# Optimization experiments

Measured on AMD Instinct MI355X. Metric: run time of the kernel, lower is better.

The kernel has to match this reference:

```python
import jax, jax.numpy as jnp
import numpy as np

N_NODES = 50000
N_EDGES = 800000
D_IN = 128
HIDDEN = 128
N_GRAPHS = 64


def gcn_conv(x, src, dst, W, b, num_nodes):
    """PyG GCNConv: out = D^{-1/2} (A+I) D^{-1/2} (x W) + b.
    src/dst already include self-loops."""
    h = x @ W  # [N, out]
    deg = jax.ops.segment_sum(jnp.ones_like(dst, dtype=h.dtype), dst,
                              num_segments=num_nodes)  # in-degree incl. self loop
    dinv = jnp.where(deg > 0, jax.lax.rsqrt(jnp.maximum(deg, 1e-12)), 0.0)
    norm = dinv[src] * dinv[dst]  # [E+N]
    msgs = h[src] * norm[:, None]  # gather + scale
    out = jax.ops.segment_sum(msgs, dst, num_segments=num_nodes)
    return out + b


def setup_inputs() -> dict:
    key = jax.random.key(0)
    ks = jax.random.split(key, 8)
    x = jax.random.normal(ks[0], (N_NODES, D_IN), dtype=jnp.float32)
    edge_index = jax.random.randint(ks[1], (2, N_EDGES), 0, N_NODES, dtype=jnp.int64)
    batch = jnp.sort(jax.random.randint(ks[2], (N_NODES,), 0, N_GRAPHS, dtype=jnp.int64))
    # Glorot-ish scaled params
    s = lambda fan_in: 1.0 / np.sqrt(fan_in)
    W1 = jax.random.normal(ks[3], (D_IN, HIDDEN), dtype=jnp.float32) * s(D_IN)
    b1 = jnp.zeros((HIDDEN,), dtype=jnp.float32)
    W2 = jax.random.normal(ks[4], (HIDDEN, HIDDEN), dtype=jnp.float32) * s(HIDDEN)
    b2 = jnp.zeros((HIDDEN,), dtype=jnp.float32)
    Wh1 = jax.random.normal(ks[5], (HIDDEN, HIDDEN), dtype=jnp.float32) * s(HIDDEN)
    bh1 = jnp.zeros((HIDDEN,), dtype=jnp.float32)
    Wh2 = jax.random.normal(ks[6], (HIDDEN, 1), dtype=jnp.float32) * s(HIDDEN)
    bh2 = jnp.zeros((1,), dtype=jnp.float32)
    return {"x": x, "edge_index": edge_index, "batch": batch,
            "W1": W1, "b1": b1, "W2": W2, "b2": b2,
            "Wh1": Wh1, "bh1": bh1, "Wh2": Wh2, "bh2": bh2}


def reference(x, edge_index, batch, W1, b1, W2, b2, Wh1, bh1, Wh2, bh2):
    n = x.shape[0]
    loop = jnp.arange(n, dtype=edge_index.dtype)
    src = jnp.concatenate([edge_index[0], loop])  # add self-loops once
    dst = jnp.concatenate([edge_index[1], loop])
    h = jax.nn.relu(gcn_conv(x, src, dst, W1, b1, n))
    h = jax.nn.relu(gcn_conv(h, src, dst, W2, b2, n))
    # global mean pool over graphs
    sums = jax.ops.segment_sum(h, batch, num_segments=N_GRAPHS)
    cnts = jax.ops.segment_sum(jnp.ones((n,), dtype=h.dtype), batch,
                               num_segments=N_GRAPHS)
    pooled = sums / jnp.maximum(cnts, 1.0)[:, None]  # [G, HIDDEN]
    # MLP head: Linear -> ReLU -> Linear -> Sigmoid -> squeeze(-1)
    z = jax.nn.relu(pooled @ Wh1 + bh1)
    out = jax.nn.sigmoid(z @ Wh2 + bh2)
    return out[:, 0]  # [G]
```

## Files before the change

### kernel.cpp

```cpp
#include <hip/hip_runtime.h>


#define NB 256
#define NBK 256

typedef __attribute__((ext_vector_type(8))) short bf16x8;
typedef __attribute__((ext_vector_type(4))) float f32x4;
typedef __attribute__((ext_vector_type(2))) float f32x2;

__device__ inline unsigned short f2bf(float f) {
    union { float f; unsigned int u; } c; c.f = f;
    unsigned int u = c.u + (0x7fffu + ((c.u >> 16) & 1u));
    return (unsigned short)(u >> 16);
}
__device__ inline float bf2f(unsigned short b) {
    union { unsigned int u; float f; } c; c.u = ((unsigned int)b) << 16;
    return c.f;
}

__device__ inline unsigned char f2fp8_sw(float f) {
    union { float f; unsigned int u; } c; c.f = f;
    unsigned int s = (c.u >> 24) & 0x80u;
    unsigned int au = c.u & 0x7FFFFFFFu;
    if (au >= 0x3C800000u) {
        if (au > 0x43E00000u) au = 0x43E00000u;
        unsigned int r = au + 0x000FFFFFu + ((au >> 20) & 1u);
        unsigned int e8 = (r >> 23) - 120u;
        unsigned int m8 = (r >> 20) & 7u;
        return (unsigned char)(s | (e8 << 3) | m8);
    }
    float av = c.f < 0.f ? -c.f : c.f;
    unsigned int M = (unsigned int)(av * 512.0f + 0.5f);
    return (unsigned char)(s | M);
}
__device__ inline float fp82f_sw(unsigned int cbyte) {
    unsigned int E = (cbyte >> 3) & 0xFu, M = cbyte & 7u;
    union { unsigned int u; float f; } v;
    v.u = ((E + 120u) << 23) | (M << 20);
    float r = E ? v.f : (float)M * 0.001953125f;
    return (cbyte & 0x80u) ? -r : r;
}

template <bool HI>
__device__ inline f32x2 fp8x2_f32(unsigned int u) {
#if __has_builtin(__builtin_amdgcn_cvt_pk_f32_fp8)
    return __builtin_amdgcn_cvt_pk_f32_fp8(u, HI);
#else
    unsigned int w = HI ? (u >> 16) : u;
    f32x2 r; r[0] = fp82f_sw(w & 0xFFu); r[1] = fp82f_sw((w >> 8) & 0xFFu);
    return r;
#endif
}
__device__ inline unsigned char f2fp8(float f) {
#if __has_builtin(__builtin_amdgcn_cvt_pk_fp8_f32)
    return (unsigned char)(__builtin_amdgcn_cvt_pk_fp8_f32(f, f, 0, false) & 0xFFu);
#else
    return f2fp8_sw(f);
#endif
}

__global__ __launch_bounds__(256) void k_hist(const int* __restrict__ dst,
                                              int* __restrict__ hist,
                                              float* __restrict__ sums,
                                              float* __restrict__ cnt,
                                              int ne, int chunk) {
    __shared__ int h[NBK];
    int t = threadIdx.x, b = blockIdx.x;
    h[t] = 0;
    int gid = b * 256 + t;
    if (gid < 64 * 128) sums[gid] = 0.0f;
    if (gid < 64) cnt[gid] = 0.0f;
    __syncthreads();
    int e0 = b * chunk, e1 = min(e0 + chunk, ne);
    for (int e = e0 + t; e < e1; e += 256) atomicAdd(&h[dst[e] >> 8], 1);
    __syncthreads();
    hist[b * NBK + t] = h[t];
}

__global__ __launch_bounds__(256) void k_scanb(int* __restrict__ hist,
                                               int* __restrict__ bstart,
                                               int* __restrict__ row_start,
                                               int n, int ne) {
    __shared__ int ps[256];
    int j = threadIdx.x;
    int run = 0;
    for (int i = 0; i < NB; ++i) {
        int t = hist[i * NBK + j];
        hist[i * NBK + j] = run;
        run += t;
    }
    ps[j] = run;
    __syncthreads();
    for (int off = 1; off < 256; off <<= 1) {
        int v = (j >= off) ? ps[j - off] : 0;
        __syncthreads();
        ps[j] += v;
        __syncthreads();
    }
    int excl = ps[j] - run;
    bstart[j] = excl;
    if (j == 255) bstart[256] = ps[255];
    if (j == 0) row_start[n] = ne;
    for (int i = 0; i < NB; ++i) hist[i * NBK + j] += excl;
}

__global__ __launch_bounds__(256) void k_scat(const int* __restrict__ src,
                                              const int* __restrict__ dst,
                                              const int* __restrict__ hist,
                                              unsigned int* __restrict__ ebuf,
                                              int ne, int chunk) {
    __shared__ int cur[NBK];
    int t = threadIdx.x, b = blockIdx.x;
    cur[t] = hist[b * NBK + t];
    __syncthreads();
    int e0 = b * chunk, e1 = min(e0 + chunk, ne);
    for (int e = e0 + t; e < e1; e += 256) {
        int d = dst[e];
        int p = atomicAdd(&cur[d >> 8], 1);
        ebuf[p] = ((unsigned int)(d & 255) << 24) | (unsigned int)src[e];
    }
}

__global__ __launch_bounds__(256) void k_bsort(const unsigned int* __restrict__ ebuf,
                                               const int* __restrict__ bstart,
                                               int* __restrict__ csr,
                                               int* __restrict__ row_start,
                                               float* __restrict__ dinv,
                                               int n) {
    __shared__ int h[NBK];
    __shared__ int sc[NBK];
    int j = threadIdx.x, b = blockIdx.x;
    int s0 = bstart[b], s1 = bstart[b + 1];
    h[j] = 0;
    __syncthreads();
    for (int e = s0 + j; e < s1; e += 256) atomicAdd(&h[ebuf[e] >> 24], 1);
    __syncthreads();
    sc[j] = h[j];
    __syncthreads();
    for (int off = 1; off < 256; off <<= 1) {
        int v = (j >= off) ? sc[j - off] : 0;
        __syncthreads();
        sc[j] += v;
        __syncthreads();
    }
    int excl = sc[j] - h[j];
    int id = b * 256 + j;
    int deg = h[j];
    if (id < n) {
        row_start[id] = s0 + excl;
        dinv[id] = rsqrtf((float)deg + 1.0f);
    }
    __syncthreads();
    h[j] = excl;
    __syncthreads();
    for (int e = s0 + j; e < s1; e += 256) {
        unsigned int pk = ebuf[e];
        int p = atomicAdd(&h[pk >> 24], 1);
        csr[s0 + p] = (int)(pk & 0x00FFFFFFu);
    }
}

__global__ __launch_bounds__(256) void k_castw(const float* __restrict__ W1,
                                               const float* __restrict__ W2,
                                               unsigned short* __restrict__ Wt1,
                                               unsigned short* __restrict__ Wt2) {
    int tid = blockIdx.x * 256 + threadIdx.x;
    int i = tid & 16383;
    int nn = i >> 7, kk = i & 127;
    if (tid < 16384) Wt1[i] = f2bf(W1[kk * 128 + nn]);
    else             Wt2[i] = f2bf(W2[kk * 128 + nn]);
}

template <bool F32IN>
__global__ __launch_bounds__(256) void k_gemm_mfma(const void* __restrict__ Xin,
                                                   const short* __restrict__ Wt,
                                                   unsigned char* __restrict__ Y8,
                                                   int n_rows) {
    int wid = threadIdx.x >> 6;
    int lane = threadIdx.x & 63;
    int r = lane & 15, q = lane >> 4;
    int m0 = blockIdx.x * 64;
    int n0 = wid * 32;

    bf16x8 bfr[2][4];
#pragma unroll
    for (int nt = 0; nt < 2; ++nt)
#pragma unroll
        for (int ks = 0; ks < 4; ++ks)
            bfr[nt][ks] = *(const bf16x8*)(Wt + (size_t)(n0 + nt * 16 + r) * 128 +
                                           ks * 32 + q * 8);

#pragma unroll
    for (int rt = 0; rt < 4; ++rt) {
        int row = m0 + rt * 16 + r;
        int rl = min(row, n_rows - 1);
        f32x4 acc0 = {0.f, 0.f, 0.f, 0.f};
        f32x4 acc1 = {0.f, 0.f, 0.f, 0.f};
#pragma unroll
        for (int ks = 0; ks < 4; ++ks) {
            bf16x8 a;
            if constexpr (F32IN) {
                const float* xr = (const float*)Xin + (size_t)rl * 128 + ks * 32 + q * 8;
                float4 f0 = *(const float4*)xr;
                float4 f1 = *(const float4*)(xr + 4);
                a[0] = (short)f2bf(f0.x); a[1] = (short)f2bf(f0.y);
                a[2] = (short)f2bf(f0.z); a[3] = (short)f2bf(f0.w);
                a[4] = (short)f2bf(f1.x); a[5] = (short)f2bf(f1.y);
                a[6] = (short)f2bf(f1.z); a[7] = (short)f2bf(f1.w);
            } else {
                a = *(const bf16x8*)((const short*)Xin + (size_t)rl * 128 + ks * 32 + q * 8);
            }
            acc0 = __builtin_amdgcn_mfma_f32_16x16x32_bf16(a, bfr[0][ks], acc0, 0, 0, 0);
            acc1 = __builtin_amdgcn_mfma_f32_16x16x32_bf16(a, bfr[1][ks], acc1, 0, 0, 0);
        }
#pragma unroll
        for (int v = 0; v < 4; ++v) {
            int orow = m0 + rt * 16 + q * 4 + v;
            if (orow < n_rows) {
                Y8[(size_t)orow * 128 + n0 + r]      = f2fp8(acc0[v]);
                Y8[(size_t)orow * 128 + n0 + 16 + r] = f2fp8(acc1[v]);
            }
        }
    }
}

__global__ __launch_bounds__(256) void k_agg(const unsigned char* __restrict__ h8,
                                             const float* __restrict__ dinv,
                                             const int* __restrict__ csr,
                                             const int* __restrict__ row_start,
                                             const float* __restrict__ bias,
                                             unsigned short* __restrict__ out,
                                             int n) {
    int node = blockIdx.x * 4 + (threadIdx.x >> 6);
    if (node >= n) return;
    int lane = threadIdx.x & 63;
    int s = lane >> 5, fi = lane & 31;
    const unsigned int* hp = (const unsigned int*)h8;

    float di = dinv[node];
    float selfw = (s == 0) ? di * di : 0.0f;
    unsigned int hu = hp[(size_t)node * 32 + fi];
    f32x2 p0 = fp8x2_f32<false>(hu);
    f32x2 p1 = fp8x2_f32<true>(hu);
    float a0 = p0[0] * selfw, a1 = p0[1] * selfw;
    float a2 = p1[0] * selfw, a3 = p1[1] * selfw;

    int beg = row_start[node];
    int end = row_start[node + 1];
    int deg = end - beg;

    int mysrc = (lane < deg) ? csr[beg + lane] : 0;
    float myw = ((lane < deg) ? dinv[mysrc] : 0.0f) * di;

    int m = min(deg, 64);
    int e = 0;
    for (; e + 8 <= m; e += 8) {
        int i0 = e + s, i1 = e + 2 + s, i2 = e + 4 + s, i3 = e + 6 + s;
        int s0 = __shfl(mysrc, i0);
        int s1 = __shfl(mysrc, i1);
        int s2 = __shfl(mysrc, i2);
        int s3 = __shfl(mysrc, i3);
        float w0 = __shfl(myw, i0);
        float w1 = __shfl(myw, i1);
        float w2 = __shfl(myw, i2);
        float w3 = __shfl(myw, i3);
        unsigned int u0 = hp[(size_t)s0 * 32 + fi];
        unsigned int u1 = hp[(size_t)s1 * 32 + fi];
        unsigned int u2 = hp[(size_t)s2 * 32 + fi];
        unsigned int u3 = hp[(size_t)s3 * 32 + fi];
        f32x2 v;
        v = fp8x2_f32<false>(u0); a0 += v[0] * w0; a1 += v[1] * w0;
        v = fp8x2_f32<true>(u0);  a2 += v[0] * w0; a3 += v[1] * w0;
        v = fp8x2_f32<false>(u1); a0 += v[0] * w1; a1 += v[1] * w1;
        v = fp8x2_f32<true>(u1);  a2 += v[0] * w1; a3 += v[1] * w1;
        v = fp8x2_f32<false>(u2); a0 += v[0] * w2; a1 += v[1] * w2;
        v = fp8x2_f32<true>(u2);  a2 += v[0] * w2; a3 += v[1] * w2;
        v = fp8x2_f32<false>(u3); a0 += v[0] * w3; a1 += v[1] * w3;
        v = fp8x2_f32<true>(u3);  a2 += v[0] * w3; a3 += v[1] * w3;
    }
    for (; e < m; e += 2) {
        int idx = e + s;
        int sx = __shfl(mysrc, idx & 63);
        float w = __shfl(myw, idx & 63);
        if (idx >= m) w = 0.0f;
        unsigned int u = hp[(size_t)sx * 32 + fi];
        f32x2 v;
        v = fp8x2_f32<false>(u); a0 += v[0] * w; a1 += v[1] * w;
        v = fp8x2_f32<true>(u);  a2 += v[0] * w; a3 += v[1] * w;
    }
    if (s == 0) {
        for (int j = beg + 64; j < end; ++j) {
            int sx = csr[j];
            float w = dinv[sx] * di;
            unsigned int u = hp[(size_t)sx * 32 + fi];
            f32x2 v;
            v = fp8x2_f32<false>(u); a0 += v[0] * w; a1 += v[1] * w;
            v = fp8x2_f32<true>(u);  a2 += v[0] * w; a3 += v[1] * w;
        }
    }

    a0 += __shfl_xor(a0, 32);
    a1 += __shfl_xor(a1, 32);
    a2 += __shfl_xor(a2, 32);
    a3 += __shfl_xor(a3, 32);

    if (s == 0) {
        float4 bv = ((const float4*)bias)[fi];
        float o0 = fmaxf(a0 + bv.x, 0.0f);
        float o1 = fmaxf(a1 + bv.y, 0.0f);
        float o2 = fmaxf(a2 + bv.z, 0.0f);
        float o3 = fmaxf(a3 + bv.w, 0.0f);
        uint2 pk;
        pk.x = (unsigned int)f2bf(o0) | ((unsigned int)f2bf(o1) << 16);
        pk.y = (unsigned int)f2bf(o2) | ((unsigned int)f2bf(o3) << 16);
        *(uint2*)(out + (size_t)node * 128 + fi * 4) = pk;
    }
}

#define POOL_CHUNK 64
__global__ __launch_bounds__(128) void k_pool(const unsigned short* __restrict__ h,
                                              const int* __restrict__ batch,
                                              float* __restrict__ sums,
                                              float* __restrict__ cnt, int n) {
    int d = threadIdx.x;
    int c0 = blockIdx.x * POOL_CHUNK;
    if (c0 >= n) return;
    int c1 = min(c0 + POOL_CHUNK, n);
    float acc = 0.f, cc = 0.f;
    int g_cur = batch[c0];
    for (int i = c0; i < c1; ++i) {
        int g = batch[i];
        if (g != g_cur) {
            atomicAdd(&sums[g_cur * 128 + d], acc);
            if (d == 0) atomicAdd(&cnt[g_cur], cc);
            acc = 0.f; cc = 0.f; g_cur = g;
        }
        acc += bf2f(h[(size_t)i * 128 + d]);
        cc += 1.f;
    }
    atomicAdd(&sums[g_cur * 128 + d], acc);
    if (d == 0) atomicAdd(&cnt[g_cur], cc);
}

__global__ __launch_bounds__(128) void k_head(const float* __restrict__ sums,
                                              const float* __restrict__ cnt,
                                              const float* __restrict__ Wh1,
                                              const float* __restrict__ bh1,
                                              const float* __restrict__ Wh2,
                                              const float* __restrict__ bh2,
                                              float* __restrict__ out) {
    int g = blockIdx.x;
    int d = threadIdx.x;
    __shared__ float sp[128];
    __shared__ float red[128];
    float c = fmaxf(cnt[g], 1.0f);
    sp[d] = sums[g * 128 + d] / c;
    __syncthreads();
    float acc = bh1[d];
    for (int k = 0; k < 128; ++k) acc += sp[k] * Wh1[k * 128 + d];
    float z = fmaxf(acc, 0.f);
    red[d] = z * Wh2[d];
    __syncthreads();
    for (int off = 64; off > 0; off >>= 1) {
        if (d < off) red[d] += red[d + off];
        __syncthreads();
    }
    if (d == 0) out[g] = 1.f / (1.f + expf(-(red[0] + bh2[0])));
}

extern "C" void kernel_launch(void* const* d_in, const int* in_sizes, int n_in,
                              void* d_out, int out_size, void* d_ws,
                              size_t ws_size, hipStream_t stream) {
    const float* x    = (const float*)d_in[0];
    const int*   ei   = (const int*)d_in[1];
    const int*   batch= (const int*)d_in[2];
    const float* W1   = (const float*)d_in[3];
    const float* b1   = (const float*)d_in[4];
    const float* W2   = (const float*)d_in[5];
    const float* b2   = (const float*)d_in[6];
    const float* Wh1  = (const float*)d_in[7];
    const float* bh1  = (const float*)d_in[8];
    const float* Wh2  = (const float*)d_in[9];
    const float* bh2  = (const float*)d_in[10];
    float* out = (float*)d_out;

    const int n  = in_sizes[0] / 128;
    const int ne = in_sizes[1] / 2;
    const int* src = ei;
    const int* dst = ei + ne;

    char* p = (char*)d_ws;
    int* hist      = (int*)p;  p += (size_t)NB * NBK * 4;
    int* bstart    = (int*)p;  p += 257 * 4;
    int* row_start = (int*)p;  p += (size_t)(n + 1) * 4;
    float* dinv    = (float*)p; p += (size_t)n * 4;
    unsigned int* ebuf = (unsigned int*)p; p += (size_t)ne * 4;
    int* csr       = (int*)p;  p += (size_t)ne * 4;
    p = (char*)(((uintptr_t)p + 15) & ~(uintptr_t)15);
    unsigned short* Wt1 = (unsigned short*)p; p += 128 * 128 * 2;
    unsigned short* Wt2 = (unsigned short*)p; p += 128 * 128 * 2;
    unsigned char* h8   = (unsigned char*)p; p += (size_t)n * 128;
    p = (char*)(((uintptr_t)p + 15) & ~(uintptr_t)15);
    unsigned short* abf = (unsigned short*)p; p += (size_t)n * 128 * 2;
    p = (char*)(((uintptr_t)p + 15) & ~(uintptr_t)15);
    float* sums = (float*)p;   p += (size_t)64 * 128 * 4;
    float* cnt  = (float*)p;

    int chunk = (ne + NB - 1) / NB;
    int nb_g = (n + 63) / 64;
    int nb_a = (n + 3) / 4;
    int nb_p = (n + POOL_CHUNK - 1) / POOL_CHUNK;

    k_hist<<<NB, 256, 0, stream>>>(dst, hist, sums, cnt, ne, chunk);
    k_scanb<<<1, 256, 0, stream>>>(hist, bstart, row_start, n, ne);
    k_scat<<<NB, 256, 0, stream>>>(src, dst, hist, ebuf, ne, chunk);
    k_bsort<<<256, 256, 0, stream>>>(ebuf, bstart, csr, row_start, dinv, n);

    k_castw<<<128, 256, 0, stream>>>(W1, W2, Wt1, Wt2);

    k_gemm_mfma<true><<<nb_g, 256, 0, stream>>>((const void*)x, (const short*)Wt1, h8, n);
    k_agg<<<nb_a, 256, 0, stream>>>(h8, dinv, csr, row_start, b1, abf, n);

    k_gemm_mfma<false><<<nb_g, 256, 0, stream>>>((const void*)abf, (const short*)Wt2, h8, n);
    k_agg<<<nb_a, 256, 0, stream>>>(h8, dinv, csr, row_start, b2, abf, n);

    k_pool<<<nb_p, 128, 0, stream>>>(abf, batch, sums, cnt, n);
    k_head<<<64, 128, 0, stream>>>(sums, cnt, Wh1, bh1, Wh2, bh2, out);
}
```

Measured before the change: 182.4 us.

## Fuse weight cast into histogram, pool into head, and pack shuffle payloads

Folds the bf16 weight transpose-cast into the histogram kernel and merges mean-pooling with the MLP head into a single per-graph kernel. The fused kernel finds each graph's node range by binary search over the sorted batch array, which removes two launches and the global atomics and zero-init of the sums buffers. The aggregation kernel now packs the source index (16 bits) and the bf16-rounded edge weight into one word, so each neighbour needs one shuffle instead of two. In exchange, node indices must fit in 16 bits, edge weights lose precision, and pooling runs on only 64 blocks, each walking its graph's rows serially.

```diff
diff --git a/kernel.cpp b/kernel.cpp
--- a/kernel.cpp
+++ b/kernel.cpp
@@ -16,6 +16,9 @@
 __device__ inline float bf2f(unsigned short b) {
     union { unsigned int u; float f; } c; c.u = ((unsigned int)b) << 16;
     return c.f;
+}
+__device__ inline float asf(unsigned int u) {
+    union { unsigned int u; float f; } c; c.u = u; return c.f;
 }
 
 __device__ inline unsigned char f2fp8_sw(float f) {
@@ -61,15 +64,22 @@
 
 __global__ __launch_bounds__(256) void k_hist(const int* __restrict__ dst,
                                               int* __restrict__ hist,
-                                              float* __restrict__ sums,
-                                              float* __restrict__ cnt,
+                                              const float* __restrict__ W1,
+                                              const float* __restrict__ W2,
+                                              unsigned short* __restrict__ Wt1,
+                                              unsigned short* __restrict__ Wt2,
                                               int ne, int chunk) {
     __shared__ int h[NBK];
     int t = threadIdx.x, b = blockIdx.x;
     h[t] = 0;
     int gid = b * 256 + t;
-    if (gid < 64 * 128) sums[gid] = 0.0f;
-    if (gid < 64) cnt[gid] = 0.0f;
+    if (b < 64) {
+        int i = gid, nn = i >> 7, kk = i & 127;
+        Wt1[i] = f2bf(W1[kk * 128 + nn]);
+    } else if (b < 128) {
+        int i = gid - 16384, nn = i >> 7, kk = i & 127;
+        Wt2[i] = f2bf(W2[kk * 128 + nn]);
+    }
     __syncthreads();
     int e0 = b * chunk, e1 = min(e0 + chunk, ne);
     for (int e = e0 + t; e < e1; e += 256) atomicAdd(&h[dst[e] >> 8], 1);
@@ -158,17 +168,6 @@
         int p = atomicAdd(&h[pk >> 24], 1);
         csr[s0 + p] = (int)(pk & 0x00FFFFFFu);
     }
-}
-
-__global__ __launch_bounds__(256) void k_castw(const float* __restrict__ W1,
-                                               const float* __restrict__ W2,
-                                               unsigned short* __restrict__ Wt1,
-                                               unsigned short* __restrict__ Wt2) {
-    int tid = blockIdx.x * 256 + threadIdx.x;
-    int i = tid & 16383;
-    int nn = i >> 7, kk = i & 127;
-    if (tid < 16384) Wt1[i] = f2bf(W1[kk * 128 + nn]);
-    else             Wt2[i] = f2bf(W2[kk * 128 + nn]);
 }
 
 template <bool F32IN>
@@ -251,23 +250,23 @@
 
     int mysrc = (lane < deg) ? csr[beg + lane] : 0;
     float myw = ((lane < deg) ? dinv[mysrc] : 0.0f) * di;
+    unsigned int mypk = ((unsigned int)f2bf(myw) << 16) | (unsigned int)(mysrc & 0xFFFF);
 
     int m = min(deg, 64);
     int e = 0;
     for (; e + 8 <= m; e += 8) {
-        int i0 = e + s, i1 = e + 2 + s, i2 = e + 4 + s, i3 = e + 6 + s;
-        int s0 = __shfl(mysrc, i0);
-        int s1 = __shfl(mysrc, i1);
-        int s2 = __shfl(mysrc, i2);
-        int s3 = __shfl(mysrc, i3);
-        float w0 = __shfl(myw, i0);
-        float w1 = __shfl(myw, i1);
-        float w2 = __shfl(myw, i2);
-        float w3 = __shfl(myw, i3);
-        unsigned int u0 = hp[(size_t)s0 * 32 + fi];
-        unsigned int u1 = hp[(size_t)s1 * 32 + fi];
-        unsigned int u2 = hp[(size_t)s2 * 32 + fi];
-        unsigned int u3 = hp[(size_t)s3 * 32 + fi];
+        unsigned int k0 = __shfl(mypk, e + s);
+        unsigned int k1 = __shfl(mypk, e + 2 + s);
+        unsigned int k2 = __shfl(mypk, e + 4 + s);
+        unsigned int k3 = __shfl(mypk, e + 6 + s);
+        unsigned int u0 = hp[(size_t)(k0 & 0xFFFFu) * 32 + fi];
+        unsigned int u1 = hp[(size_t)(k1 & 0xFFFFu) * 32 + fi];
+        unsigned int u2 = hp[(size_t)(k2 & 0xFFFFu) * 32 + fi];
+        unsigned int u3 = hp[(size_t)(k3 & 0xFFFFu) * 32 + fi];
+        float w0 = asf(k0 & 0xFFFF0000u);
+        float w1 = asf(k1 & 0xFFFF0000u);
+        float w2 = asf(k2 & 0xFFFF0000u);
+        float w3 = asf(k3 & 0xFFFF0000u);
         f32x2 v;
         v = fp8x2_f32<false>(u0); a0 += v[0] * w0; a1 += v[1] * w0;
         v = fp8x2_f32<true>(u0);  a2 += v[0] * w0; a3 += v[1] * w0;
@@ -280,10 +279,10 @@
     }
     for (; e < m; e += 2) {
         int idx = e + s;
-        int sx = __shfl(mysrc, idx & 63);
-        float w = __shfl(myw, idx & 63);
+        unsigned int k = __shfl(mypk, idx & 63);
+        float w = asf(k & 0xFFFF0000u);
         if (idx >= m) w = 0.0f;
-        unsigned int u = hp[(size_t)sx * 32 + fi];
+        unsigned int u = hp[(size_t)(k & 0xFFFFu) * 32 + fi];
         f32x2 v;
         v = fp8x2_f32<false>(u); a0 += v[0] * w; a1 += v[1] * w;
         v = fp8x2_f32<true>(u);  a2 += v[0] * w; a3 += v[1] * w;
@@ -317,55 +316,48 @@
     }
 }
 
-#define POOL_CHUNK 64
-__global__ __launch_bounds__(128) void k_pool(const unsigned short* __restrict__ h,
-                                              const int* __restrict__ batch,
-                                              float* __restrict__ sums,
-                                              float* __restrict__ cnt, int n) {
-    int d = threadIdx.x;
-    int c0 = blockIdx.x * POOL_CHUNK;
-    if (c0 >= n) return;
-    int c1 = min(c0 + POOL_CHUNK, n);
-    float acc = 0.f, cc = 0.f;
-    int g_cur = batch[c0];
-    for (int i = c0; i < c1; ++i) {
-        int g = batch[i];
-        if (g != g_cur) {
-            atomicAdd(&sums[g_cur * 128 + d], acc);
-            if (d == 0) atomicAdd(&cnt[g_cur], cc);
-            acc = 0.f; cc = 0.f; g_cur = g;
-        }
+__global__ __launch_bounds__(256) void k_phead(const unsigned short* __restrict__ h,
+                                               const int* __restrict__ batch,
+                                               const float* __restrict__ Wh1,
+                                               const float* __restrict__ bh1,
+                                               const float* __restrict__ Wh2,
+                                               const float* __restrict__ bh2,
+                                               float* __restrict__ out, int n) {
+    int g = blockIdx.x;
+    int t = threadIdx.x;
+    int d = t & 127, half = t >> 7;
+
+    int lo, hi;
+    { int a = 0, b = n; while (a < b) { int m = (a + b) >> 1; if (batch[m] < g) a = m + 1; else b = m; } lo = a; }
+    { int a = lo, b = n; while (a < b) { int m = (a + b) >> 1; if (batch[m] < g + 1) a = m + 1; else b = m; } hi = a; }
+
+    float acc = 0.f;
+    for (int i = lo + half; i < hi; i += 2)
         acc += bf2f(h[(size_t)i * 128 + d]);
-        cc += 1.f;
-    }
-    atomicAdd(&sums[g_cur * 128 + d], acc);
-    if (d == 0) atomicAdd(&cnt[g_cur], cc);
-}
-
-__global__ __launch_bounds__(128) void k_head(const float* __restrict__ sums,
-                                              const float* __restrict__ cnt,
-                                              const float* __restrict__ Wh1,
-                                              const float* __restrict__ bh1,
-                                              const float* __restrict__ Wh2,
-                                              const float* __restrict__ bh2,
-                                              float* __restrict__ out) {
-    int g = blockIdx.x;
-    int d = threadIdx.x;
+
+    __shared__ float red[256];
     __shared__ float sp[128];
-    __shared__ float red[128];
-    float c = fmaxf(cnt[g], 1.0f);
-    sp[d] = sums[g * 128 + d] / c;
-    __syncthreads();
-    float acc = bh1[d];
-    for (int k = 0; k < 128; ++k) acc += sp[k] * Wh1[k * 128 + d];
-    float z = fmaxf(acc, 0.f);
-    red[d] = z * Wh2[d];
+    red[t] = acc;
+    __syncthreads();
+    if (t < 128) {
+        float c = fmaxf((float)(hi - lo), 1.0f);
+        sp[t] = (red[t] + red[t + 128]) / c;
+    }
+    __syncthreads();
+
+    float z = 0.f;
+    if (t < 128) {
+        float a2 = bh1[t];
+        for (int k = 0; k < 128; ++k) a2 += sp[k] * Wh1[k * 128 + t];
+        z = fmaxf(a2, 0.f) * Wh2[t];
+    }
+    red[t] = (t < 128) ? z : 0.f;
     __syncthreads();
     for (int off = 64; off > 0; off >>= 1) {
-        if (d < off) red[d] += red[d + off];
+        if (t < off) red[t] += red[t + off];
         __syncthreads();
     }
-    if (d == 0) out[g] = 1.f / (1.f + expf(-(red[0] + bh2[0])));
+    if (t == 0) out[g] = 1.f / (1.f + expf(-(red[0] + bh2[0])));
 }
 
 extern "C" void kernel_launch(void* const* d_in, const int* in_sizes, int n_in,
@@ -402,28 +394,21 @@
     unsigned char* h8   = (unsigned char*)p; p += (size_t)n * 128;
     p = (char*)(((uintptr_t)p + 15) & ~(uintptr_t)15);
     unsigned short* abf = (unsigned short*)p; p += (size_t)n * 128 * 2;
-    p = (char*)(((uintptr_t)p + 15) & ~(uintptr_t)15);
-    float* sums = (float*)p;   p += (size_t)64 * 128 * 4;
-    float* cnt  = (float*)p;
 
     int chunk = (ne + NB - 1) / NB;
     int nb_g = (n + 63) / 64;
     int nb_a = (n + 3) / 4;
-    int nb_p = (n + POOL_CHUNK - 1) / POOL_CHUNK;
-
-    k_hist<<<NB, 256, 0, stream>>>(dst, hist, sums, cnt, ne, chunk);
+
+    k_hist<<<NB, 256, 0, stream>>>(dst, hist, W1, W2, Wt1, Wt2, ne, chunk);
     k_scanb<<<1, 256, 0, stream>>>(hist, bstart, row_start, n, ne);
     k_scat<<<NB, 256, 0, stream>>>(src, dst, hist, ebuf, ne, chunk);
     k_bsort<<<256, 256, 0, stream>>>(ebuf, bstart, csr, row_start, dinv, n);
 
-    k_castw<<<128, 256, 0, stream>>>(W1, W2, Wt1, Wt2);
-
     k_gemm_mfma<true><<<nb_g, 256, 0, stream>>>((const void*)x, (const short*)Wt1, h8, n);
     k_agg<<<nb_a, 256, 0, stream>>>(h8, dinv, csr, row_start, b1, abf, n);
 
     k_gemm_mfma<false><<<nb_g, 256, 0, stream>>>((const void*)abf, (const short*)Wt2, h8, n);
     k_agg<<<nb_a, 256, 0, stream>>>(h8, dinv, csr, row_start, b2, abf, n);
 
-    k_pool<<<nb_p, 128, 0, stream>>>(abf, batch, sums, cnt, n);
-    k_head<<<64, 128, 0, stream>>>(sums, cnt, Wh1, bh1, Wh2, bh2, out);
-}
+    k_phead<<<64, 256, 0, stream>>>(abf, batch, Wh1, bh1, Wh2, bh2, out, n);
+}
```

Measured after the change: 265.7 us. 1.46x slower.
